# Optimization experiments

Hardware: AMD Instinct MI355X
Metric: run time of the kernel (lower is better)

The kernel has to match this reference:

```python
import jax, jax.numpy as jnp
import numpy as np

NUM_EMBEDDINGS = 1024
EMBEDDING_DIM = 256
COMMITMENT_COST = 0.25
STRAIGHT_THROUGH = True


def setup_inputs() -> dict:
    key = jax.random.key(0)
    k_in, k_emb = jax.random.split(key)
    inputs = jax.random.normal(k_in, (32, 32, 32, EMBEDDING_DIM), dtype=jnp.float32)
    # variance_scaling(1.0, 'fan_in', 'uniform') over (K, D): limit = sqrt(3 / fan_in)
    limit = np.sqrt(3.0 / EMBEDDING_DIM).astype(np.float32)
    embedding = jax.random.uniform(
        k_emb, (NUM_EMBEDDINGS, EMBEDDING_DIM), dtype=jnp.float32,
        minval=-limit, maxval=limit)
    return {"inputs": inputs, "embedding": embedding}


def reference(inputs, embedding):
    input_shape = inputs.shape
    flat = jnp.reshape(inputs, (-1, EMBEDDING_DIM))  # [N, D]
    # squared euclidean distances [N, K]
    distances = (jnp.sum(flat ** 2, axis=1, keepdims=True)
                 - 2.0 * jnp.matmul(flat, embedding.T)
                 + jnp.sum(embedding ** 2, axis=1)[None, :])
    encoding_indices = jnp.argmin(distances, axis=1)  # [N]
    quantized = jnp.take(embedding, encoding_indices, axis=0)  # [N, D] gather == one-hot matmul
    quantized = jnp.reshape(quantized, input_shape)
    if STRAIGHT_THROUGH:
        quantized = inputs + jax.lax.stop_gradient(quantized - inputs)
    else:
        quantized = jax.lax.stop_gradient(quantized)
    e_latent_loss = jnp.mean((jax.lax.stop_gradient(quantized) - inputs) ** 2)
    q_latent_loss = jnp.mean((quantized - jax.lax.stop_gradient(inputs)) ** 2)
    vq_loss = q_latent_loss + COMMITMENT_COST * e_latent_loss
    return quantized, vq_loss, encoding_indices
```

## Files before the change

kernel.cpp:

```cpp
#include <hip/hip_runtime.h>

#define NPTS 32768
#define DIM 256
#define KCODES 1024
#define NSPLIT 8
#define BN 256
#define BKC 128
#define BK 64
#define MARGIN 0.08f
#define CVT_BLOCKS 2048

typedef __attribute__((ext_vector_type(8))) short short8v;
typedef __attribute__((ext_vector_type(8))) unsigned short ushort8v;
typedef __attribute__((ext_vector_type(4))) float f32x4;

static __device__ __forceinline__ unsigned short f2bf(float f) {
    unsigned int u = __float_as_uint(f);
    unsigned int r = (u + 0x7fffu + ((u >> 16) & 1u)) >> 16;
    return (unsigned short)r;
}

static __device__ __forceinline__ void gload16(const void* g, void* l) {
    __builtin_amdgcn_global_load_lds((const __attribute__((address_space(1))) void*)g,
                                     (__attribute__((address_space(3))) void*)l, 16, 0, 0);
}

__global__ void convert_kernel(const float* __restrict__ X, const float* __restrict__ E,
                               unsigned short* __restrict__ Xb, unsigned short* __restrict__ Eb,
                               float* __restrict__ Cnp, float* __restrict__ xsq_part,
                               int* __restrict__ counters) {
#pragma clang fp contract(off)
    const int tid = threadIdx.x;
    if (blockIdx.x == 0 && tid == 0) { counters[0] = 0; counters[32] = 0; }
    if (blockIdx.x >= CVT_BLOCKS) {
        int k = (blockIdx.x - CVT_BLOCKS) * 256 + tid;
        const float* e = E + (size_t)k * DIM;
        float half[2];
        for (int h = 0; h < 2; ++h) {
            const float* b = e + h * 128;
            float s[8];
#pragma unroll
            for (int j = 0; j < 8; ++j) { float v = b[j]; s[j] = v * v; }
            for (int i = 8; i < 128; i += 8) {
#pragma unroll
                for (int j = 0; j < 8; ++j) { float v = b[i + j]; s[j] += v * v; }
            }
            half[h] = ((s[0] + s[1]) + (s[2] + s[3])) + ((s[4] + s[5]) + (s[6] + s[7]));
        }
        Cnp[k] = half[0] + half[1];
        return;
    }
    const int total = (NPTS + KCODES) * DIM / 8;
    float xsq = 0.f;
    for (int i = blockIdx.x * 256 + tid; i < total; i += CVT_BLOCKS * 256) {
        size_t e8 = (size_t)i * 8;
        const float* src; unsigned short* dst; size_t off;
        bool isX = e8 < (size_t)NPTS * DIM;
        if (isX) { src = X; dst = Xb; off = e8; }
        else { src = E; dst = Eb; off = e8 - (size_t)NPTS * DIM; }
        float4 f0 = *(const float4*)(src + off);
        float4 f1 = *(const float4*)(src + off + 4);
        ushort8v v;
        v[0] = f2bf(f0.x); v[1] = f2bf(f0.y); v[2] = f2bf(f0.z); v[3] = f2bf(f0.w);
        v[4] = f2bf(f1.x); v[5] = f2bf(f1.y); v[6] = f2bf(f1.z); v[7] = f2bf(f1.w);
        *(ushort8v*)(dst + off) = v;
        if (isX)
            xsq += f0.x * f0.x + f0.y * f0.y + f0.z * f0.z + f0.w * f0.w
                 + f1.x * f1.x + f1.y * f1.y + f1.z * f1.z + f1.w * f1.w;
    }
    __shared__ float red[256];
    red[tid] = xsq;
    __syncthreads();
#pragma unroll
    for (int s = 128; s > 0; s >>= 1) {
        if (tid < s) red[tid] += red[tid + s];
        __syncthreads();
    }
    if (tid == 0) xsq_part[blockIdx.x] = red[0];
}

__global__ __launch_bounds__(256, 2) void dist_kernel(
        const unsigned short* __restrict__ Xb, const unsigned short* __restrict__ Eb,
        const float* __restrict__ Cnp,
        float* __restrict__ ws_m1, unsigned int* __restrict__ cand) {
    __shared__ unsigned short xs[BN * BK];
    __shared__ unsigned short es[BKC * BK];

    const int tid = threadIdx.x;
    const int lane = tid & 63;
    const int wave = tid >> 6;
    const int lg = lane >> 4, lc = lane & 15;
    const int pbase = blockIdx.x * BN;
    const int split = blockIdx.y;
    const int cbase = split * BKC;

    f32x4 acc[4][8];
#pragma unroll
    for (int i = 0; i < 4; ++i)
#pragma unroll
        for (int j = 0; j < 8; ++j) acc[i][j] = (f32x4){0.f, 0.f, 0.f, 0.f};

    for (int ks = 0; ks < DIM / BK; ++ks) {
        const int k0 = ks * BK;
        __syncthreads();
#pragma unroll
        for (int q = 0; q < 8; ++q) {
            const int B = wave * 8192 + q * 1024 + lane * 16;
            const int row = B >> 7;
            const int cs = ((B >> 4) & 7) ^ (row & 7);
            gload16(Xb + (size_t)(pbase + row) * DIM + k0 + cs * 8,
                    (char*)xs + wave * 8192 + q * 1024);
        }
#pragma unroll
        for (int q = 0; q < 4; ++q) {
            const int B = wave * 4096 + q * 1024 + lane * 16;
            const int row = B >> 7;
            const int cs = ((B >> 4) & 7) ^ (row & 7);
            gload16(Eb + (size_t)(cbase + row) * DIM + k0 + cs * 8,
                    (char*)es + wave * 4096 + q * 1024);
        }
        __syncthreads();
#pragma unroll
        for (int kk = 0; kk < 2; ++kk) {
            short8v a[4];
#pragma unroll
            for (int f = 0; f < 4; ++f) {
                int row = wave * 64 + f * 16 + lc;
                int cs = (kk * 4 + lg) ^ (row & 7);
                a[f] = *(const short8v*)&xs[row * BK + cs * 8];
            }
#pragma unroll
            for (int j = 0; j < 8; ++j) {
                int row = j * 16 + lc;
                int cs = (kk * 4 + lg) ^ (row & 7);
                short8v b = *(const short8v*)&es[row * BK + cs * 8];
#pragma unroll
                for (int i = 0; i < 4; ++i)
                    acc[i][j] = __builtin_amdgcn_mfma_f32_16x16x32_bf16(a[i], b, acc[i][j], 0, 0, 0);
            }
        }
    }

    float en8[8];
#pragma unroll
    for (int j = 0; j < 8; ++j) en8[j] = Cnp[cbase + j * 16 + lc];

    float m1[4][4];
#pragma unroll
    for (int i = 0; i < 4; ++i)
#pragma unroll
        for (int r = 0; r < 4; ++r) m1[i][r] = 3.4e38f;
#pragma unroll
    for (int j = 0; j < 8; ++j)
#pragma unroll
        for (int i = 0; i < 4; ++i)
#pragma unroll
            for (int r = 0; r < 4; ++r)
                m1[i][r] = fminf(m1[i][r], __builtin_fmaf(-2.f, acc[i][j][r], en8[j]));
#pragma unroll
    for (int m = 1; m < 16; m <<= 1)
#pragma unroll
        for (int i = 0; i < 4; ++i)
#pragma unroll
            for (int r = 0; r < 4; ++r)
                m1[i][r] = fminf(m1[i][r], __shfl_xor(m1[i][r], m));

#pragma unroll
    for (int i = 0; i < 4; ++i)
#pragma unroll
        for (int r = 0; r < 4; ++r) {
            float thr = m1[i][r] + MARGIN;
            unsigned int sl[8];
#pragma unroll
            for (int j = 0; j < 8; ++j) {
                float d = __builtin_fmaf(-2.f, acc[i][j][r], en8[j]);
                unsigned long long mm = __ballot(d <= thr);
                sl[j] = (unsigned int)((mm >> (lg * 16)) & 0xFFFFull);
            }
            if (lc == 0) {
                int p = pbase + wave * 64 + i * 16 + lg * 4 + r;
                uint4 w4 = { sl[0] | (sl[1] << 16), sl[2] | (sl[3] << 16),
                             sl[4] | (sl[5] << 16), sl[6] | (sl[7] << 16) };
                *(uint4*)&cand[((size_t)p * NSPLIT + split) * 4] = w4;
                ws_m1[(size_t)p * NSPLIT + split] = m1[i][r];
            }
        }
}

__global__ void resolve_kernel(const float* __restrict__ ws_m1, const unsigned int* __restrict__ cand,
                               int* __restrict__ final_idx, int* __restrict__ list,
                               int* __restrict__ counters,
                               const float* __restrict__ xsq_part, float* __restrict__ v1_part,
                               float* __restrict__ out_loss) {
    const int tid = threadIdx.x;
    const int p = blockIdx.x * 256 + tid;
    float4 ma = *(const float4*)&ws_m1[(size_t)p * NSPLIT];
    float4 mb = *(const float4*)&ws_m1[(size_t)p * NSPLIT + 4];
    float m[8] = { ma.x, ma.y, ma.z, ma.w, mb.x, mb.y, mb.z, mb.w };
    float v1 = m[0]; int sstar = 0;
#pragma unroll
    for (int s = 1; s < NSPLIT; ++s)
        if (m[s] < v1) { v1 = m[s]; sstar = s; }
    float thr = v1 + MARGIN;
    bool flag = false;
#pragma unroll
    for (int s = 0; s < NSPLIT; ++s)
        if (s != sstar && m[s] <= thr) flag = true;
    uint4 w4 = *(const uint4*)&cand[((size_t)p * NSPLIT + sstar) * 4];
    int pc = __builtin_popcount(w4.x) + __builtin_popcount(w4.y)
           + __builtin_popcount(w4.z) + __builtin_popcount(w4.w);
    flag = flag || (pc > 1);
    int idx;
    if (w4.x)      idx = __builtin_ctz(w4.x);
    else if (w4.y) idx = 32 + __builtin_ctz(w4.y);
    else if (w4.z) idx = 64 + __builtin_ctz(w4.z);
    else           idx = 96 + __builtin_ctz(w4.w);
    final_idx[p] = sstar * BKC + idx;
    if (flag) {
        int slot = atomicAdd(&counters[0], 1);
        list[slot] = p;
    }

    __shared__ float red[256];
    red[tid] = v1;
    __syncthreads();
#pragma unroll
    for (int s = 128; s > 0; s >>= 1) {
        if (tid < s) red[tid] += red[tid + s];
        __syncthreads();
    }
    if (tid == 0) v1_part[blockIdx.x] = red[0];

    __shared__ int amlast;
    if (tid == 0) {
        __threadfence();
        amlast = (atomicAdd(&counters[32], 1) == (int)gridDim.x - 1);
    }
    __syncthreads();
    if (amlast) {
        __threadfence();
        double s = 0.0;
        for (int i = tid; i < CVT_BLOCKS; i += 256) s += (double)xsq_part[i];
        for (int i = tid; i < NPTS / 256; i += 256) s += (double)v1_part[i];
        __shared__ double dred[256];
        dred[tid] = s;
        __syncthreads();
#pragma unroll
        for (int t = 128; t > 0; t >>= 1) {
            if (tid < t) dred[tid] += dred[tid + t];
            __syncthreads();
        }
        if (tid == 0)
            out_loss[0] = (float)(1.25 * dred[0] / (double)((size_t)NPTS * DIM));
    }
}

__global__ __launch_bounds__(256) void rescore_np_kernel(
        const float* __restrict__ X, const float* __restrict__ E,
        const float* __restrict__ Cnp, const unsigned int* __restrict__ cand,
        const int* __restrict__ list, const int* __restrict__ counters,
        int* __restrict__ final_idx) {
#pragma clang fp contract(off)
    const int tid = threadIdx.x;
    const int lane = tid & 63;
    const int wave = tid >> 6;
    const int cnt = counters[0];
    __shared__ float xsh[4][DIM];

    for (int base = blockIdx.x * 4; base < cnt; base += gridDim.x * 4) {
        const int li = base + wave;
        const bool active = (li < cnt);
        const int p = list[active ? li : (cnt - 1)];
        __syncthreads();
        *(float4*)&xsh[wave][lane * 4] = *(const float4*)(X + (size_t)p * DIM + lane * 4);
        __syncthreads();

        float s = 0.f;
        if (lane < 16) {
            const int h = lane >> 3, j = lane & 7;
            float v = xsh[wave][h * 128 + j];
            s = v * v;
            for (int i = 8; i < 128; i += 8) {
                float w = xsh[wave][h * 128 + i + j];
                s += w * w;
            }
        }
        float t0 = __shfl(s, 0), t1 = __shfl(s, 1), t2 = __shfl(s, 2), t3 = __shfl(s, 3);
        float t4 = __shfl(s, 4), t5 = __shfl(s, 5), t6 = __shfl(s, 6), t7 = __shfl(s, 7);
        float u0 = __shfl(s, 8), u1 = __shfl(s, 9), u2 = __shfl(s, 10), u3 = __shfl(s, 11);
        float u4 = __shfl(s, 12), u5 = __shfl(s, 13), u6 = __shfl(s, 14), u7 = __shfl(s, 15);
        const float A = (((t0 + t1) + (t2 + t3)) + ((t4 + t5) + (t6 + t7)))
                      + (((u0 + u1) + (u2 + u3)) + ((u4 + u5) + (u6 + u7)));

        float bv = 3.4e38f; int bi = 0x7FFFFFFF;
        if (lane < 32) {
            unsigned int bits = cand[(size_t)p * 32 + lane];
            const int cb = (lane >> 2) * 128 + (lane & 3) * 32;
            while (bits) {
                int t = __builtin_ctz(bits);
                bits &= bits - 1;
                int c = cb + t;
                const float4* er4 = (const float4*)(E + (size_t)c * DIM);
                float acc = 0.f;
                for (int d4 = 0; d4 < DIM / 4; ++d4) {
                    float4 e4 = er4[d4];
                    float4 x4 = *(const float4*)&xsh[wave][d4 * 4];
                    acc = __builtin_fmaf(x4.x, e4.x, acc);
                    acc = __builtin_fmaf(x4.y, e4.y, acc);
                    acc = __builtin_fmaf(x4.z, e4.z, acc);
                    acc = __builtin_fmaf(x4.w, e4.w, acc);
                }
                float tt = A - 2.0f * acc;
                float dnp = tt + Cnp[c];
                if (dnp < bv) { bv = dnp; bi = c; }
            }
        }
#pragma unroll
        for (int m = 1; m < 64; m <<= 1) {
            float ov = __shfl_xor(bv, m);
            int oi = __shfl_xor(bi, m);
            if (ov < bv || (ov == bv && oi < bi)) { bv = ov; bi = oi; }
        }
        if (active && lane == 0) final_idx[p] = bi;
    }
}

__global__ void gather_kernel(const float* __restrict__ E, const int* __restrict__ final_idx,
                              float* __restrict__ out_q, float* __restrict__ out_idx) {
    const int tid = threadIdx.x;
    const int p = blockIdx.x * 16 + (tid >> 4);
    const int c = tid & 15;
    const int bi = final_idx[p];
#pragma unroll
    for (int k = 0; k < 4; ++k) {
        int d4 = c + k * 16;
        float4 e4 = *(const float4*)(E + (size_t)bi * DIM + d4 * 4);
        *(float4*)(out_q + (size_t)p * DIM + d4 * 4) = e4;
    }
    if (c == 0) out_idx[p] = (float)bi;
}

extern "C" void kernel_launch(void* const* d_in, const int* in_sizes, int n_in,
                              void* d_out, int out_size, void* d_ws, size_t ws_size,
                              hipStream_t stream) {
    const float* X = (const float*)d_in[0];
    const float* E = (const float*)d_in[1];
    float* out = (float*)d_out;
    float* out_q = out;
    float* out_loss = out + (size_t)NPTS * DIM;
    float* out_idx = out + (size_t)NPTS * DIM + 1;

    unsigned short* Xb = (unsigned short*)d_out;
    unsigned short* Eb = Xb + (size_t)NPTS * DIM;
    unsigned int* cand = (unsigned int*)(Eb + (size_t)KCODES * DIM);

    float* ws = (float*)d_ws;
    float* Cnp = ws;
    float* ws_m1 = Cnp + KCODES;
    int* final_idx = (int*)(ws_m1 + (size_t)NPTS * NSPLIT);
    int* counters = final_idx + NPTS;
    int* list = counters + 64;
    float* xsq_part = (float*)(list + NPTS);
    float* v1_part = xsq_part + CVT_BLOCKS;

    convert_kernel<<<CVT_BLOCKS + KCODES / 256, 256, 0, stream>>>(X, E, Xb, Eb, Cnp,
                                                                  xsq_part, counters);
    dist_kernel<<<dim3(NPTS / BN, NSPLIT), 256, 0, stream>>>(Xb, Eb, Cnp, ws_m1, cand);
    resolve_kernel<<<NPTS / 256, 256, 0, stream>>>(ws_m1, cand, final_idx, list, counters,
                                                   xsq_part, v1_part, out_loss);
    rescore_np_kernel<<<512, 256, 0, stream>>>(X, E, Cnp, cand, list, counters, final_idx);
    gather_kernel<<<NPTS / 16, 256, 0, stream>>>(E, final_idx, out_q, out_idx);
}
```

Before: 89.69 us.

## Fuse ambiguous-point rescoring into resolve kernel with block-local candidate lists

```diff
diff --git a/kernel.cpp b/kernel.cpp
--- a/kernel.cpp
+++ b/kernel.cpp
@@ -187,13 +187,30 @@
         }
 }
 
-__global__ void resolve_kernel(const float* __restrict__ ws_m1, const unsigned int* __restrict__ cand,
-                               int* __restrict__ final_idx, int* __restrict__ list,
-                               int* __restrict__ counters,
-                               const float* __restrict__ xsq_part, float* __restrict__ v1_part,
-                               float* __restrict__ out_loss) {
+__global__ __launch_bounds__(256) void resolve_kernel(
+        const float* __restrict__ ws_m1, const unsigned int* __restrict__ cand,
+        const float* __restrict__ X, const float* __restrict__ E,
+        const float* __restrict__ Cnp, int* __restrict__ counters,
+        const float* __restrict__ xsq_part, float* __restrict__ v1_part,
+        float* __restrict__ out_loss, int* __restrict__ final_idx) {
+#pragma clang fp contract(off)
     const int tid = threadIdx.x;
-    const int p = blockIdx.x * 256 + tid;
+    const int lane = tid & 63;
+    const int wave = tid >> 6;
+    const int pblk = blockIdx.x * 256;
+    const int p = pblk + tid;
+
+    __shared__ float xsh[4][DIM];
+    __shared__ int fidx[256];
+    __shared__ int llist[256];
+    __shared__ int lcnt;
+    __shared__ float red[256];
+    __shared__ double dred[256];
+    __shared__ int amlast;
+
+    if (tid == 0) lcnt = 0;
+    __syncthreads();
+
     float4 ma = *(const float4*)&ws_m1[(size_t)p * NSPLIT];
     float4 mb = *(const float4*)&ws_m1[(size_t)p * NSPLIT + 4];
     float m[8] = { ma.x, ma.y, ma.z, ma.w, mb.x, mb.y, mb.z, mb.w };
@@ -215,13 +232,12 @@
     else if (w4.y) idx = 32 + __builtin_ctz(w4.y);
     else if (w4.z) idx = 64 + __builtin_ctz(w4.z);
     else           idx = 96 + __builtin_ctz(w4.w);
-    final_idx[p] = sstar * BKC + idx;
+    fidx[tid] = sstar * BKC + idx;
     if (flag) {
-        int slot = atomicAdd(&counters[0], 1);
-        list[slot] = p;
-    }
-
-    __shared__ float red[256];
+        int slot = atomicAdd(&lcnt, 1);
+        llist[slot] = tid;
+    }
+
     red[tid] = v1;
     __syncthreads();
 #pragma unroll
@@ -231,7 +247,6 @@
     }
     if (tid == 0) v1_part[blockIdx.x] = red[0];
 
-    __shared__ int amlast;
     if (tid == 0) {
         __threadfence();
         amlast = (atomicAdd(&counters[32], 1) == (int)gridDim.x - 1);
@@ -242,7 +257,6 @@
         double s = 0.0;
         for (int i = tid; i < CVT_BLOCKS; i += 256) s += (double)xsq_part[i];
         for (int i = tid; i < NPTS / 256; i += 256) s += (double)v1_part[i];
-        __shared__ double dred[256];
         dred[tid] = s;
         __syncthreads();
 #pragma unroll
@@ -253,26 +267,14 @@
         if (tid == 0)
             out_loss[0] = (float)(1.25 * dred[0] / (double)((size_t)NPTS * DIM));
     }
-}
-
-__global__ __launch_bounds__(256) void rescore_np_kernel(
-        const float* __restrict__ X, const float* __restrict__ E,
-        const float* __restrict__ Cnp, const unsigned int* __restrict__ cand,
-        const int* __restrict__ list, const int* __restrict__ counters,
-        int* __restrict__ final_idx) {
-#pragma clang fp contract(off)
-    const int tid = threadIdx.x;
-    const int lane = tid & 63;
-    const int wave = tid >> 6;
-    const int cnt = counters[0];
-    __shared__ float xsh[4][DIM];
-
-    for (int base = blockIdx.x * 4; base < cnt; base += gridDim.x * 4) {
+
+    for (int base = 0; base < lcnt; base += 4) {
         const int li = base + wave;
-        const bool active = (li < cnt);
-        const int p = list[active ? li : (cnt - 1)];
-        __syncthreads();
-        *(float4*)&xsh[wave][lane * 4] = *(const float4*)(X + (size_t)p * DIM + lane * 4);
+        const bool active = (li < lcnt);
+        const int pl = llist[active ? li : (lcnt - 1)];
+        const int pg = pblk + pl;
+        __syncthreads();
+        *(float4*)&xsh[wave][lane * 4] = *(const float4*)(X + (size_t)pg * DIM + lane * 4);
         __syncthreads();
 
         float s = 0.f;
@@ -294,7 +296,7 @@
 
         float bv = 3.4e38f; int bi = 0x7FFFFFFF;
         if (lane < 32) {
-            unsigned int bits = cand[(size_t)p * 32 + lane];
+            unsigned int bits = cand[(size_t)pg * 32 + lane];
             const int cb = (lane >> 2) * 128 + (lane & 3) * 32;
             while (bits) {
                 int t = __builtin_ctz(bits);
@@ -316,13 +318,16 @@
             }
         }
 #pragma unroll
-        for (int m = 1; m < 64; m <<= 1) {
-            float ov = __shfl_xor(bv, m);
-            int oi = __shfl_xor(bi, m);
+        for (int mm = 1; mm < 64; mm <<= 1) {
+            float ov = __shfl_xor(bv, mm);
+            int oi = __shfl_xor(bi, mm);
             if (ov < bv || (ov == bv && oi < bi)) { bv = ov; bi = oi; }
         }
-        if (active && lane == 0) final_idx[p] = bi;
-    }
+        if (active && lane == 0) fidx[pl] = bi;
+    }
+    __syncthreads();
+
+    final_idx[p] = fidx[tid];
 }
 
 __global__ void gather_kernel(const float* __restrict__ E, const int* __restrict__ final_idx,
@@ -359,15 +364,13 @@
     float* ws_m1 = Cnp + KCODES;
     int* final_idx = (int*)(ws_m1 + (size_t)NPTS * NSPLIT);
     int* counters = final_idx + NPTS;
-    int* list = counters + 64;
-    float* xsq_part = (float*)(list + NPTS);
+    float* xsq_part = (float*)(counters + 64);
     float* v1_part = xsq_part + CVT_BLOCKS;
 
     convert_kernel<<<CVT_BLOCKS + KCODES / 256, 256, 0, stream>>>(X, E, Xb, Eb, Cnp,
                                                                   xsq_part, counters);
     dist_kernel<<<dim3(NPTS / BN, NSPLIT), 256, 0, stream>>>(Xb, Eb, Cnp, ws_m1, cand);
-    resolve_kernel<<<NPTS / 256, 256, 0, stream>>>(ws_m1, cand, final_idx, list, counters,
-                                                   xsq_part, v1_part, out_loss);
-    rescore_np_kernel<<<512, 256, 0, stream>>>(X, E, Cnp, cand, list, counters, final_idx);
+    resolve_kernel<<<NPTS / 256, 256, 0, stream>>>(ws_m1, cand, X, E, Cnp, counters,
+                                                   xsq_part, v1_part, out_loss, final_idx);
     gather_kernel<<<NPTS / 16, 256, 0, stream>>>(E, final_idx, out_q, out_idx);
 }
```

Result: slower. 152.5 us (+70.0%).

## Rescore flagged candidates as flat (point, code) pairs with atomicMin keys

Applied to the files above, without the earlier changes.

```diff
diff --git a/kernel.cpp b/kernel.cpp
--- a/kernel.cpp
+++ b/kernel.cpp
@@ -9,6 +9,7 @@
 #define BK 64
 #define MARGIN 0.08f
 #define CVT_BLOCKS 2048
+#define MAXPAIRS (2500000)
 
 typedef __attribute__((ext_vector_type(8))) short short8v;
 typedef __attribute__((ext_vector_type(8))) unsigned short ushort8v;
@@ -188,8 +189,8 @@
 }
 
 __global__ void resolve_kernel(const float* __restrict__ ws_m1, const unsigned int* __restrict__ cand,
-                               int* __restrict__ final_idx, int* __restrict__ list,
-                               int* __restrict__ counters,
+                               unsigned long long* __restrict__ keymin,
+                               unsigned int* __restrict__ pairs, int* __restrict__ counters,
                                const float* __restrict__ xsq_part, float* __restrict__ v1_part,
                                float* __restrict__ out_loss) {
     const int tid = threadIdx.x;
@@ -215,10 +216,34 @@
     else if (w4.y) idx = 32 + __builtin_ctz(w4.y);
     else if (w4.z) idx = 64 + __builtin_ctz(w4.z);
     else           idx = 96 + __builtin_ctz(w4.w);
-    final_idx[p] = sstar * BKC + idx;
-    if (flag) {
-        int slot = atomicAdd(&counters[0], 1);
-        list[slot] = p;
+
+    if (!flag) {
+        keymin[p] = (unsigned long long)(sstar * BKC + idx);
+    } else {
+        keymin[p] = ~0ULL;
+        uint4 wb[8]; int tot = 0;
+#pragma unroll
+        for (int s = 0; s < NSPLIT; ++s) {
+            wb[s] = *(const uint4*)&cand[((size_t)p * NSPLIT + s) * 4];
+            tot += __builtin_popcount(wb[s].x) + __builtin_popcount(wb[s].y)
+                 + __builtin_popcount(wb[s].z) + __builtin_popcount(wb[s].w);
+        }
+        int slot = atomicAdd(&counters[0], tot);
+#pragma unroll
+        for (int s = 0; s < NSPLIT; ++s) {
+            unsigned int ww[4] = { wb[s].x, wb[s].y, wb[s].z, wb[s].w };
+#pragma unroll
+            for (int w = 0; w < 4; ++w) {
+                unsigned int bits = ww[w];
+                while (bits) {
+                    int t = __builtin_ctz(bits);
+                    bits &= bits - 1;
+                    int c = s * BKC + w * 32 + t;
+                    if (slot < MAXPAIRS) pairs[slot] = ((unsigned)p << 10) | (unsigned)c;
+                    ++slot;
+                }
+            }
+        }
     }
 
     __shared__ float red[256];
@@ -255,82 +280,60 @@
     }
 }
 
-__global__ __launch_bounds__(256) void rescore_np_kernel(
+__global__ __launch_bounds__(256) void rescore_pairs_kernel(
         const float* __restrict__ X, const float* __restrict__ E,
-        const float* __restrict__ Cnp, const unsigned int* __restrict__ cand,
-        const int* __restrict__ list, const int* __restrict__ counters,
-        int* __restrict__ final_idx) {
+        const float* __restrict__ Cnp, const unsigned int* __restrict__ pairs,
+        const int* __restrict__ counters, unsigned long long* __restrict__ keymin) {
 #pragma clang fp contract(off)
-    const int tid = threadIdx.x;
-    const int lane = tid & 63;
-    const int wave = tid >> 6;
-    const int cnt = counters[0];
-    __shared__ float xsh[4][DIM];
-
-    for (int base = blockIdx.x * 4; base < cnt; base += gridDim.x * 4) {
-        const int li = base + wave;
-        const bool active = (li < cnt);
-        const int p = list[active ? li : (cnt - 1)];
-        __syncthreads();
-        *(float4*)&xsh[wave][lane * 4] = *(const float4*)(X + (size_t)p * DIM + lane * 4);
-        __syncthreads();
-
-        float s = 0.f;
-        if (lane < 16) {
-            const int h = lane >> 3, j = lane & 7;
-            float v = xsh[wave][h * 128 + j];
-            s = v * v;
-            for (int i = 8; i < 128; i += 8) {
-                float w = xsh[wave][h * 128 + i + j];
-                s += w * w;
-            }
-        }
-        float t0 = __shfl(s, 0), t1 = __shfl(s, 1), t2 = __shfl(s, 2), t3 = __shfl(s, 3);
-        float t4 = __shfl(s, 4), t5 = __shfl(s, 5), t6 = __shfl(s, 6), t7 = __shfl(s, 7);
-        float u0 = __shfl(s, 8), u1 = __shfl(s, 9), u2 = __shfl(s, 10), u3 = __shfl(s, 11);
-        float u4 = __shfl(s, 12), u5 = __shfl(s, 13), u6 = __shfl(s, 14), u7 = __shfl(s, 15);
-        const float A = (((t0 + t1) + (t2 + t3)) + ((t4 + t5) + (t6 + t7)))
-                      + (((u0 + u1) + (u2 + u3)) + ((u4 + u5) + (u6 + u7)));
-
-        float bv = 3.4e38f; int bi = 0x7FFFFFFF;
-        if (lane < 32) {
-            unsigned int bits = cand[(size_t)p * 32 + lane];
-            const int cb = (lane >> 2) * 128 + (lane & 3) * 32;
-            while (bits) {
-                int t = __builtin_ctz(bits);
-                bits &= bits - 1;
-                int c = cb + t;
-                const float4* er4 = (const float4*)(E + (size_t)c * DIM);
-                float acc = 0.f;
-                for (int d4 = 0; d4 < DIM / 4; ++d4) {
-                    float4 e4 = er4[d4];
-                    float4 x4 = *(const float4*)&xsh[wave][d4 * 4];
-                    acc = __builtin_fmaf(x4.x, e4.x, acc);
-                    acc = __builtin_fmaf(x4.y, e4.y, acc);
-                    acc = __builtin_fmaf(x4.z, e4.z, acc);
-                    acc = __builtin_fmaf(x4.w, e4.w, acc);
-                }
-                float tt = A - 2.0f * acc;
-                float dnp = tt + Cnp[c];
-                if (dnp < bv) { bv = dnp; bi = c; }
-            }
-        }
-#pragma unroll
-        for (int m = 1; m < 64; m <<= 1) {
-            float ov = __shfl_xor(bv, m);
-            int oi = __shfl_xor(bi, m);
-            if (ov < bv || (ov == bv && oi < bi)) { bv = ov; bi = oi; }
-        }
-        if (active && lane == 0) final_idx[p] = bi;
-    }
-}
-
-__global__ void gather_kernel(const float* __restrict__ E, const int* __restrict__ final_idx,
+    const int np = min(counters[0], MAXPAIRS);
+    for (int i = blockIdx.x * 256 + threadIdx.x; i < np; i += gridDim.x * 256) {
+        const unsigned int pr = pairs[i];
+        const int p = pr >> 10;
+        const int c = pr & 1023;
+        const float* x = X + (size_t)p * DIM;
+
+        float half[2];
+        for (int h = 0; h < 2; ++h) {
+            const float* b = x + h * 128;
+            float s[8];
+#pragma unroll
+            for (int j = 0; j < 8; ++j) { float v = b[j]; s[j] = v * v; }
+            for (int i8 = 8; i8 < 128; i8 += 8) {
+#pragma unroll
+                for (int j = 0; j < 8; ++j) { float v = b[i8 + j]; s[j] += v * v; }
+            }
+            half[h] = ((s[0] + s[1]) + (s[2] + s[3])) + ((s[4] + s[5]) + (s[6] + s[7]));
+        }
+        const float A = half[0] + half[1];
+
+        const float4* er4 = (const float4*)(E + (size_t)c * DIM);
+        const float4* xr4 = (const float4*)x;
+        float acc = 0.f;
+        for (int d4 = 0; d4 < DIM / 4; ++d4) {
+            float4 e4 = er4[d4];
+            float4 x4 = xr4[d4];
+            acc = __builtin_fmaf(x4.x, e4.x, acc);
+            acc = __builtin_fmaf(x4.y, e4.y, acc);
+            acc = __builtin_fmaf(x4.z, e4.z, acc);
+            acc = __builtin_fmaf(x4.w, e4.w, acc);
+        }
+        float tt = A - 2.0f * acc;
+        float dnp = tt + Cnp[c];
+
+        unsigned int ub = __float_as_uint(dnp);
+        unsigned int sk = (ub & 0x80000000u) ? ~ub : (ub | 0x80000000u);
+        unsigned long long key = ((unsigned long long)sk << 32) | (unsigned)c;
+        atomicMin(&keymin[p], key);
+    }
+}
+
+__global__ void gather_kernel(const float* __restrict__ E,
+                              const unsigned long long* __restrict__ keymin,
                               float* __restrict__ out_q, float* __restrict__ out_idx) {
     const int tid = threadIdx.x;
     const int p = blockIdx.x * 16 + (tid >> 4);
     const int c = tid & 15;
-    const int bi = final_idx[p];
+    const int bi = (int)(keymin[p] & 1023ULL);
 #pragma unroll
     for (int k = 0; k < 4; ++k) {
         int d4 = c + k * 16;
@@ -353,21 +356,22 @@
     unsigned short* Xb = (unsigned short*)d_out;
     unsigned short* Eb = Xb + (size_t)NPTS * DIM;
     unsigned int* cand = (unsigned int*)(Eb + (size_t)KCODES * DIM);
+    unsigned int* pairs = cand + (size_t)NPTS * NSPLIT * 4;
 
     float* ws = (float*)d_ws;
     float* Cnp = ws;
     float* ws_m1 = Cnp + KCODES;
-    int* final_idx = (int*)(ws_m1 + (size_t)NPTS * NSPLIT);
-    int* counters = final_idx + NPTS;
-    int* list = counters + 64;
-    float* xsq_part = (float*)(list + NPTS);
+    int* counters = (int*)(ws_m1 + (size_t)NPTS * NSPLIT);
+    float* xsq_part = (float*)(counters + 64);
     float* v1_part = xsq_part + CVT_BLOCKS;
+    unsigned long long* keymin =
+        (unsigned long long*)(((size_t)(v1_part + NPTS / 256) + 7) & ~(size_t)7);
 
     convert_kernel<<<CVT_BLOCKS + KCODES / 256, 256, 0, stream>>>(X, E, Xb, Eb, Cnp,
                                                                   xsq_part, counters);
     dist_kernel<<<dim3(NPTS / BN, NSPLIT), 256, 0, stream>>>(Xb, Eb, Cnp, ws_m1, cand);
-    resolve_kernel<<<NPTS / 256, 256, 0, stream>>>(ws_m1, cand, final_idx, list, counters,
+    resolve_kernel<<<NPTS / 256, 256, 0, stream>>>(ws_m1, cand, keymin, pairs, counters,
                                                    xsq_part, v1_part, out_loss);
-    rescore_np_kernel<<<512, 256, 0, stream>>>(X, E, Cnp, cand, list, counters, final_idx);
-    gather_kernel<<<NPTS / 16, 256, 0, stream>>>(E, final_idx, out_q, out_idx);
-}
+    rescore_pairs_kernel<<<512, 256, 0, stream>>>(X, E, Cnp, pairs, counters, keymin);
+    gather_kernel<<<NPTS / 16, 256, 0, stream>>>(E, keymin, out_q, out_idx);
+}
```

Result: no change. 87.96 us, median of 2 (-1.9%).
